# Kernel optimization log

Hardware: AMD Instinct MI355X
Metric: run time of the kernel (lower is better)

The kernel has to match this reference:

```python
import jax, jax.numpy as jnp
import numpy as np
from jax import lax

B_SZ = 2
EMBED = 384          # d_model == d_inner (expand=1)
DEPTH = 12
DSTATE = 16
DCONV = 4
DTRANK = 24          # ceil(384/16)
GH, GW, GD = 16, 8, 8
PH, PW, PD = 16, 32, 8
L = GH * GW * GD            # 1024 tokens
PATCH_DIM = PH * PW * PD    # 4096


def setup_inputs() -> dict:
    key = jax.random.key(0)
    ks = jax.random.split(key, 12)
    d = EMBED
    return {
        "x": jax.random.normal(ks[0], (B_SZ, 1, GH * PH, GW * PW, GD * PD), dtype=jnp.float32),
        "batch_params": jax.random.uniform(ks[1], (B_SZ, 4), minval=0.1, maxval=1.0),
        "patch_w": jax.random.normal(ks[2], (PATCH_DIM, d)) * 0.02,
        "patch_b": jnp.zeros((d,), jnp.float32),
        "in_proj_w": jax.random.normal(ks[3], (DEPTH, d, 2 * d)) * 0.02,
        "conv_w": jax.random.normal(ks[4], (DEPTH, d, DCONV)) * 0.1,
        "conv_b": jnp.zeros((DEPTH, d), jnp.float32),
        "x_proj_w": jax.random.normal(ks[5], (DEPTH, d, DTRANK + 2 * DSTATE)) * 0.02,
        "dt_proj_w": jax.random.normal(ks[6], (DEPTH, DTRANK, d)) * 0.02,
        "dt_proj_b": jnp.full((DEPTH, d), -4.6, jnp.float32),  # softplus(-4.6) ~ 0.01 init dt
        "A_log": jnp.log(jnp.tile(jnp.arange(1, DSTATE + 1, dtype=jnp.float32), (DEPTH, EMBED, 1))),
        "Dskip": jnp.ones((DEPTH, d), jnp.float32),
        "out_proj_w": jax.random.normal(ks[7], (DEPTH, d, d)) * 0.02,
        "norm_w": jnp.ones((DEPTH, d), jnp.float32),
        "norm_b": jnp.zeros((DEPTH, d), jnp.float32),
        "final_norm_w": jnp.ones((d,), jnp.float32),
        "final_norm_b": jnp.zeros((d,), jnp.float32),
        "has_velocity_mask": jnp.array([True, False]),
    }


def _layernorm(h, w, b, eps=1e-5):
    mu = h.mean(-1, keepdims=True)
    var = ((h - mu) ** 2).mean(-1, keepdims=True)
    return (h - mu) / jnp.sqrt(var + eps) * w + b


def _physical_coords(batch_params, mask):
    # grid indices -> physical (distance, angle, velocity/time), [B, L, 3]
    h = jnp.arange(GH, dtype=jnp.float32)[None, :, None, None]
    w = jnp.arange(GW, dtype=jnp.float32)[None, None, :, None]
    dd = jnp.arange(GD, dtype=jnp.float32)[None, None, None, :]
    rr = batch_params[:, 0][:, None, None, None]
    ar = batch_params[:, 1][:, None, None, None]
    vr = batch_params[:, 2][:, None, None, None]
    B = batch_params.shape[0]
    shape = (B, GH, GW, GD)
    dist = jnp.broadcast_to(h * rr, shape)
    angle = jnp.broadcast_to((w - GW / 2) * ar, shape)
    m = mask[:, None, None, None]
    vel = jnp.broadcast_to(jnp.where(m, (dd - GD / 2) * vr, dd * vr), shape)
    coords = jnp.stack([dist, angle, vel], axis=-1).reshape(B, -1, 3)
    # PIPE normalization
    d0 = coords[:, :, 0]
    dmax = jnp.max(d0, 1, keepdims=True)
    n0 = d0 / jnp.where(dmax == 0, 1.0, dmax)
    a = coords[:, :, 1]
    amax = jnp.max(jnp.abs(a), 1, keepdims=True)
    n1 = a / jnp.where(amax == 0, 1.0, amax)
    v = coords[:, :, 2]
    vam = jnp.max(jnp.abs(v), 1, keepdims=True)
    vam = jnp.where(vam == 0, 1.0, vam)
    vm = jnp.max(v, 1, keepdims=True)
    vm = jnp.where(vm == 0, 1.0, vm)
    n2 = jnp.where(mask[:, None], v / vam, v / vm)
    return jnp.stack([n0, n1, n2], axis=-1)


def _pos_embed(coords):
    # embed_dim % 3 == 0 and per-coord dim even -> pure sin/cos blocks
    dpc = EMBED // 3
    omega = 1.0 / (10000.0 ** (jnp.arange(dpc // 2, dtype=jnp.float32) / (dpc / 2.0)))
    embs = []
    for j in range(3):
        out = coords[:, :, j, None] * omega          # [B, L, dpc//2]
        embs.append(jnp.concatenate([jnp.sin(out), jnp.cos(out)], axis=-1))
    return jnp.concatenate(embs, axis=-1)            # [B, L, EMBED]


def _forward(x, batch_params, patch_w, patch_b, in_proj_w, conv_w, conv_b,
             x_proj_w, dt_proj_w, dt_proj_b, A_log, Dskip, out_proj_w,
             norm_w, norm_b, final_norm_w, final_norm_b, has_velocity_mask):
    B = x.shape[0]
    # 3D patch embed (conv3d with stride == kernel == patch) as reshape + GEMM
    xp = x[:, 0].reshape(B, GH, PH, GW, PW, GD, PD)
    xp = xp.transpose(0, 1, 3, 5, 2, 4, 6).reshape(B, L, PATCH_DIM)
    tok = xp @ patch_w + patch_b                     # [B, L, EMBED]
    coords = _physical_coords(batch_params, has_velocity_mask)
    tok = tok + _pos_embed(coords)

    def mamba_layer(tok, params):
        ipw, cw, cb, xpw, dtw, dtb, Al, Dp, opw, nw, nb = params
        h = _layernorm(tok, nw, nb)
        xz = h @ ipw                                  # [B, L, 2d]
        xi, z = jnp.split(xz, 2, axis=-1)
        # depthwise causal conv1d (kernel DCONV) + silu
        xc = lax.conv_general_dilated(
            xi.transpose(0, 2, 1), cw[:, None, :], (1,), [(DCONV - 1, 0)],
            feature_group_count=EMBED, dimension_numbers=("NCH", "OIH", "NCH"))
        xc = jax.nn.silu(xc + cb[:, None]).transpose(0, 2, 1)   # [B, L, d]
        dbl = xc @ xpw
        dt = jax.nn.softplus(dbl[..., :DTRANK] @ dtw + dtb)     # [B, L, d]
        Bm = dbl[..., DTRANK:DTRANK + DSTATE]                   # [B, L, N]
        Cm = dbl[..., DTRANK + DSTATE:]                         # [B, L, N]
        A = -jnp.exp(Al)                                        # [d, N]

        def step(hst, inps):
            dt_t, B_t, C_t, u_t = inps                          # [B,d],[B,N],[B,N],[B,d]
            dA = jnp.exp(dt_t[:, :, None] * A)                  # [B, d, N]
            hst = hst * dA + (dt_t * u_t)[:, :, None] * B_t[:, None, :]
            return hst, jnp.einsum("bdn,bn->bd", hst, C_t)

        h0 = jnp.zeros((B, EMBED, DSTATE), tok.dtype)
        _, ys = lax.scan(step, h0, (dt.transpose(1, 0, 2), Bm.transpose(1, 0, 2),
                                    Cm.transpose(1, 0, 2), xc.transpose(1, 0, 2)))
        y = ys.transpose(1, 0, 2) + xc * Dp
        y = y * jax.nn.silu(z)
        return tok + y @ opw, None

    tok, _ = lax.scan(mamba_layer, tok,
                      (in_proj_w, conv_w, conv_b, x_proj_w, dt_proj_w, dt_proj_b,
                       A_log, Dskip, out_proj_w, norm_w, norm_b))
    return _layernorm(tok, final_norm_w, final_norm_b)


def reference(x, batch_params, patch_w, patch_b, in_proj_w, conv_w, conv_b,
              x_proj_w, dt_proj_w, dt_proj_b, A_log, Dskip, out_proj_w,
              norm_w, norm_b, final_norm_w, final_norm_b, has_velocity_mask):
    return _forward(x, batch_params, patch_w, patch_b, in_proj_w, conv_w, conv_b,
                    x_proj_w, dt_proj_w, dt_proj_b, A_log, Dskip, out_proj_w,
                    norm_w, norm_b, final_norm_w, final_norm_b, has_velocity_mask)
```

## Files before the change

kernel.cpp:

```cpp
#include <hip/hip_runtime.h>


#define NTOK 2048

typedef short bf16x8 __attribute__((ext_vector_type(8)));
typedef float f32x4 __attribute__((ext_vector_type(4)));
typedef unsigned short us4 __attribute__((ext_vector_type(4)));

__device__ __forceinline__ float bf2f(unsigned short u) {
    return __uint_as_float(((unsigned)u) << 16);
}
__device__ __forceinline__ unsigned short f2bf(float f) {
    unsigned u = __float_as_uint(f);
    u += 0x7fffu + ((u >> 16) & 1u);
    return (unsigned short)(u >> 16);
}
__device__ __forceinline__ float siluf(float x) { return x / (1.f + expf(-x)); }

__device__ __forceinline__ float ldr(const void* p, size_t i, int bf) {
    if (bf) return bf2f(((const unsigned short*)p)[i]);
    return ((const float*)p)[i];
}
template<int BF>
__device__ __forceinline__ float ld(const void* p, size_t i) {
    if (BF) return bf2f(((const unsigned short*)p)[i]);
    return ((const float*)p)[i];
}

__global__ void detect_kernel(const void* dskip, int* flag) {
    flag[0] = (((const unsigned short*)dskip)[0] == 0x3F80u) ? 1 : 0;
}

__global__ __launch_bounds__(256)
void transposeP_kernel(const int* flag, const void* pw, unsigned short* wtP)
{
    __shared__ unsigned short Ts[32 * 36];
    const int bid = blockIdx.x;
    const int kb = bid / 12, nb = bid % 12;
    const int tid = threadIdx.x;
    const int r = tid >> 3, c0 = (tid & 7) * 4;
    const int BF = *flag;
#pragma unroll
    for (int i = 0; i < 4; i++) {
        size_t si = (size_t)(kb * 32 + r) * 384 + nb * 32 + c0 + i;
        Ts[(c0 + i) * 36 + r] = f2bf(ldr(pw, si, BF));
    }
    __syncthreads();
    *(us4*)(wtP + (size_t)(nb * 32 + r) * 4096 + kb * 32 + c0) = *(const us4*)&Ts[r * 36 + c0];
}

__global__ __launch_bounds__(256)
void transposeL_kernel(const int* flag, const void* ipw, const void* opw, int lyr,
                       unsigned short* wtL, unsigned short* wtOl)
{
    __shared__ unsigned short Ts[32 * 36];
    const int bid = blockIdx.x;
    const void* src; size_t soff; unsigned short* dst; int N, kb, nb;
    if (bid < 288) {
        src = ipw; soff = (size_t)lyr * 294912; dst = wtL; N = 768;
        kb = bid / 24; nb = bid % 24;
    } else {
        int rel = bid - 288;
        src = opw; soff = (size_t)lyr * 147456; dst = wtOl; N = 384;
        kb = rel / 12; nb = rel % 12;
    }
    const int tid = threadIdx.x;
    const int r = tid >> 3, c0 = (tid & 7) * 4;
    const int BF = *flag;
#pragma unroll
    for (int i = 0; i < 4; i++) {
        size_t si = soff + (size_t)(kb * 32 + r) * N + nb * 32 + c0 + i;
        Ts[(c0 + i) * 36 + r] = f2bf(ldr(src, si, BF));
    }
    __syncthreads();
    *(us4*)(dst + (size_t)(nb * 32 + r) * 384 + kb * 32 + c0) = *(const us4*)&Ts[r * 36 + c0];
}

__global__ __launch_bounds__(256)
void transposeAll_kernel(const int* flag, const void* ipw, const void* opw,
                         unsigned short* wtL12, unsigned short* wtO12)
{
    __shared__ unsigned short Ts[32 * 36];
    const int lyr = blockIdx.y;
    const int bid = blockIdx.x;
    const void* src; size_t soff; unsigned short* dst; int N, kb, nb;
    if (bid < 288) {
        src = ipw; soff = (size_t)lyr * 294912;
        dst = wtL12 + (size_t)lyr * 294912; N = 768;
        kb = bid / 24; nb = bid % 24;
    } else {
        int rel = bid - 288;
        src = opw; soff = (size_t)lyr * 147456;
        dst = wtO12 + (size_t)lyr * 147456; N = 384;
        kb = rel / 12; nb = rel % 12;
    }
    const int tid = threadIdx.x;
    const int r = tid >> 3, c0 = (tid & 7) * 4;
    const int BF = *flag;
#pragma unroll
    for (int i = 0; i < 4; i++) {
        size_t si = soff + (size_t)(kb * 32 + r) * N + nb * 32 + c0 + i;
        Ts[(c0 + i) * 36 + r] = f2bf(ldr(src, si, BF));
    }
    __syncthreads();
    *(us4*)(dst + (size_t)(nb * 32 + r) * 384 + kb * 32 + c0) = *(const us4*)&Ts[r * 36 + c0];
}


template<int MODE>
__global__ __launch_bounds__(256)
void gemm_kernel(const unsigned short* __restrict__ A,
                 const unsigned short* __restrict__ WT,
                 void* __restrict__ out0, unsigned short* __restrict__ out1)
{
    const int mtile = blockIdx.x;
    const int ntile = blockIdx.y;
    const int tid = threadIdx.x;
    const int w = tid >> 6, lane = tid & 63;
    const int l15 = lane & 15, quad = lane >> 4;
    const int mbase = mtile * 64 + (w & 1) * 32;
    const int nbase = ntile * 64 + (w >> 1) * 32;
    f32x4 acc00 = {0.f,0.f,0.f,0.f}, acc01 = acc00, acc10 = acc00, acc11 = acc00;
    const bf16x8* Ap0 = (const bf16x8*)(A + (size_t)(mbase + l15) * 384 + quad * 8);
    const bf16x8* Ap1 = (const bf16x8*)(A + (size_t)(mbase + 16 + l15) * 384 + quad * 8);
    const bf16x8* Bp0 = (const bf16x8*)(WT + (size_t)(nbase + l15) * 384 + quad * 8);
    const bf16x8* Bp1 = (const bf16x8*)(WT + (size_t)(nbase + 16 + l15) * 384 + quad * 8);
    const int nkt = (MODE == 1) ? 6 : 12;
    const int kt0 = (MODE == 1) ? blockIdx.z * 6 : 0;
#pragma unroll
    for (int ki = 0; ki < nkt; ki++) {
        const int kt = kt0 + ki;
        bf16x8 a0 = Ap0[kt * 4];
        bf16x8 a1 = Ap1[kt * 4];
        bf16x8 b0 = Bp0[kt * 4];
        bf16x8 b1 = Bp1[kt * 4];
        acc00 = __builtin_amdgcn_mfma_f32_16x16x32_bf16(a0, b0, acc00, 0, 0, 0);
        acc01 = __builtin_amdgcn_mfma_f32_16x16x32_bf16(a0, b1, acc01, 0, 0, 0);
        acc10 = __builtin_amdgcn_mfma_f32_16x16x32_bf16(a1, b0, acc10, 0, 0, 0);
        acc11 = __builtin_amdgcn_mfma_f32_16x16x32_bf16(a1, b1, acc11, 0, 0, 0);
    }
    f32x4 accs[2][2] = {{acc00, acc01}, {acc10, acc11}};
#pragma unroll
    for (int mi = 0; mi < 2; mi++)
#pragma unroll
    for (int ni = 0; ni < 2; ni++)
#pragma unroll
    for (int r = 0; r < 4; r++) {
        int m = mbase + mi * 16 + quad * 4 + r;
        int n = nbase + ni * 16 + l15;
        float v = accs[mi][ni][r];
        if (MODE == 0) {
            if (n < 384) ((unsigned short*)out0)[(size_t)m * 384 + n] = f2bf(v);
            else out1[(size_t)m * 384 + (n - 384)] = f2bf(siluf(v));
        } else {
            atomicAdd(&((float*)out0)[(size_t)m * 384 + n], v);
        }
    }
}

template<int BF>
__device__ void posinit_body(const void* __restrict__ pb, const void* __restrict__ bparams,
                             const unsigned char* __restrict__ maskp, float* __restrict__ tok)
{
    const int gid = blockIdx.x * 256 + threadIdx.x;
    const int t = gid / 384;
    const int n = gid - t * 384;
    const int b = t >> 10, l = t & 1023;
    const int gh = l >> 6, gw = (l >> 3) & 7, gd = l & 7;
    const int j = n >> 7;
    const int ii = n & 127;
    const int i0 = (ii < 64) ? ii : ii - 64;
    const float omega = exp2f(-(float)i0 * 0.20762050593046014f);
    float rr = ld<BF>(bparams, b * 4 + 0);
    float ar = ld<BF>(bparams, b * 4 + 1);
    float vr = ld<BF>(bparams, b * 4 + 2);
    bool mk = maskp[b] != 0;
    float cj;
    if (j == 0) {
        float dmax = (rr >= 0.f) ? 15.f * rr : 0.f;
        if (dmax == 0.f) dmax = 1.f;
        cj = (float)gh * rr / dmax;
    } else if (j == 1) {
        float amax = 4.f * fabsf(ar);
        if (amax == 0.f) amax = 1.f;
        cj = (float)(gw - 4) * ar / amax;
    } else {
        if (mk) {
            float dmx = 4.f * fabsf(vr);
            if (dmx == 0.f) dmx = 1.f;
            cj = (float)(gd - 4) * vr / dmx;
        } else {
            float dmx = (vr >= 0.f) ? 7.f * vr : 0.f;
            if (dmx == 0.f) dmx = 1.f;
            cj = (float)gd * vr / dmx;
        }
    }
    float s = cj * omega;
    float pos = (ii < 64) ? sinf(s) : cosf(s);
    tok[gid] = ld<BF>(pb, n) + pos;
}

__global__ __launch_bounds__(256)
void posinit_kernel(const int* flag, const void* pb, const void* bparams,
                    const unsigned char* maskp, float* tok)
{
    if (*flag) posinit_body<1>(pb, bparams, maskp, tok);
    else       posinit_body<0>(pb, bparams, maskp, tok);
}

template<int BF>
__device__ void patch_body(const void* __restrict__ x,
                           const unsigned short* __restrict__ WT,
                           float* __restrict__ tok, short* __restrict__ As)
{
    const int mtile = blockIdx.x;
    const int ntile = blockIdx.y;
    const int kz = blockIdx.z;
    const int tid = threadIdx.x;
    const int w = tid >> 6, lane = tid & 63;
    const int l15 = lane & 15, quad = lane >> 4;
    const int nbase = ntile * 64 + (w >> 1) * 32;
    const int mrow0 = (w & 1) * 32 + l15;
    f32x4 acc00 = {0.f,0.f,0.f,0.f}, acc01 = acc00, acc10 = acc00, acc11 = acc00;
#pragma unroll
    for (int p2 = 0; p2 < 2; p2++) {
        const int plane = kz * 2 + p2;
        if (p2) __syncthreads();
        {
            const int pw = lane >> 1;
            const int pd4 = (lane & 1) * 4;
#pragma unroll
            for (int i = 0; i < 16; i++) {
                int r = i * 4 + w;
                int t = mtile * 64 + r;
                int bb = t >> 10, l = t & 1023;
                int gh = l >> 6, gw = (l >> 3) & 7, gd = l & 7;
                size_t base = (size_t)bb * 4194304u + (size_t)gh * 262144u
                            + (size_t)gw * 2048u + (size_t)gd * 8u
                            + (size_t)plane * 16384u + (size_t)pw * 64u + (size_t)pd4;
                short* dst = As + r * 260 + lane * 4;
                if (BF) {
                    *(us4*)dst = *(const us4*)((const unsigned short*)x + base);
                } else {
                    float4 p4 = *(const float4*)((const float*)x + base);
                    dst[0] = (short)f2bf(p4.x); dst[1] = (short)f2bf(p4.y);
                    dst[2] = (short)f2bf(p4.z); dst[3] = (short)f2bf(p4.w);
                }
            }
        }
        __syncthreads();
        const bf16x8* Bp0 = (const bf16x8*)(WT + (size_t)(nbase + l15) * 4096
                                            + plane * 256 + quad * 8);
        const bf16x8* Bp1 = (const bf16x8*)(WT + (size_t)(nbase + 16 + l15) * 4096
                                            + plane * 256 + quad * 8);
#pragma unroll
        for (int kt = 0; kt < 8; kt++) {
            const short* a0p = As + mrow0 * 260 + kt * 32 + quad * 8;
            const short* a1p = a0p + 16 * 260;
            bf16x8 a0, a1;
            {
                us4 lo = *(const us4*)a0p, hi = *(const us4*)(a0p + 4);
                a0[0]=lo[0]; a0[1]=lo[1]; a0[2]=lo[2]; a0[3]=lo[3];
                a0[4]=hi[0]; a0[5]=hi[1]; a0[6]=hi[2]; a0[7]=hi[3];
                us4 lo1 = *(const us4*)a1p, hi1 = *(const us4*)(a1p + 4);
                a1[0]=lo1[0]; a1[1]=lo1[1]; a1[2]=lo1[2]; a1[3]=lo1[3];
                a1[4]=hi1[0]; a1[5]=hi1[1]; a1[6]=hi1[2]; a1[7]=hi1[3];
            }
            bf16x8 b0 = Bp0[kt * 4];
            bf16x8 b1 = Bp1[kt * 4];
            acc00 = __builtin_amdgcn_mfma_f32_16x16x32_bf16(a0, b0, acc00, 0, 0, 0);
            acc01 = __builtin_amdgcn_mfma_f32_16x16x32_bf16(a0, b1, acc01, 0, 0, 0);
            acc10 = __builtin_amdgcn_mfma_f32_16x16x32_bf16(a1, b0, acc10, 0, 0, 0);
            acc11 = __builtin_amdgcn_mfma_f32_16x16x32_bf16(a1, b1, acc11, 0, 0, 0);
        }
    }
    f32x4 accs[2][2] = {{acc00, acc01}, {acc10, acc11}};
#pragma unroll
    for (int mi = 0; mi < 2; mi++)
#pragma unroll
    for (int ni = 0; ni < 2; ni++) {
        int n = nbase + ni * 16 + l15;
#pragma unroll
        for (int r = 0; r < 4; r++) {
            int m = mtile * 64 + (w & 1) * 32 + mi * 16 + quad * 4 + r;
            atomicAdd(&tok[(size_t)m * 384 + n], accs[mi][ni][r]);
        }
    }
}

__global__ __launch_bounds__(256)
void patch_kernel(const int* flag, const void* x, const unsigned short* wtP, float* tok)
{
    __shared__ short As[64 * 260];
    if (*flag) patch_body<1>(x, wtP, tok, As);
    else       patch_body<0>(x, wtP, tok, As);
}

__global__ __launch_bounds__(64)
void ln_kernel(const int* flag, const float* __restrict__ in, const void* __restrict__ w,
               const void* __restrict__ b, int woff, void* __restrict__ out, int obf)
{
    const int BF = *flag;
    const int wbf = obf | BF;
    const int t = blockIdx.x;
    const int lane = threadIdx.x;
    float v[6];
    float s = 0.f;
#pragma unroll
    for (int i = 0; i < 6; i++) { v[i] = in[(size_t)t * 384 + lane + 64 * i]; s += v[i]; }
#pragma unroll
    for (int o = 1; o < 64; o <<= 1) s += __shfl_xor(s, o);
    const float mu = s * (1.f / 384.f);
    float s2 = 0.f;
#pragma unroll
    for (int i = 0; i < 6; i++) { float d = v[i] - mu; s2 += d * d; }
#pragma unroll
    for (int o = 1; o < 64; o <<= 1) s2 += __shfl_xor(s2, o);
    const float rstd = rsqrtf(s2 * (1.f / 384.f) + 1e-5f);
#pragma unroll
    for (int i = 0; i < 6; i++) {
        int c = lane + 64 * i;
        float o = (v[i] - mu) * rstd * ldr(w, woff + c, BF) + ldr(b, woff + c, BF);
        if (wbf) ((unsigned short*)out)[(size_t)t * 384 + c] = f2bf(o);
        else     ((float*)out)[(size_t)t * 384 + c] = o;
    }
}

template<int BF>
__device__ void convfused_body(float* xcs, float* dblA,
                          const unsigned short* __restrict__ xi,
                          const void* __restrict__ cw, const void* __restrict__ cb,
                          const void* __restrict__ xpw, const void* __restrict__ dtw,
                          const void* __restrict__ dtbp, int lyr,
                          unsigned short* __restrict__ xc, unsigned short* __restrict__ dtv,
                          float* __restrict__ Bm, float* __restrict__ Cm)
{
    const int tb = blockIdx.x * 4;
    const int tid = threadIdx.x;
    const size_t cwo = (size_t)lyr * 1536;
    const size_t cbo = (size_t)lyr * 384;
    const size_t xpo = (size_t)lyr * 21504;
    const size_t dto = (size_t)lyr * 9216;
#pragma unroll
    for (int i = 0; i < 6; i++) {
        int p = i * 256 + tid;
        int tl = p / 384, c = p - tl * 384;
        int t = tb + tl;
        int b = t >> 10, l = t & 1023;
        float acc = ld<BF>(cb, cbo + c);
#pragma unroll
        for (int jj = 0; jj < 4; jj++) {
            int ls = l - 3 + jj;
            if (ls >= 0)
                acc = fmaf(bf2f(xi[(size_t)((b << 10) + ls) * 384 + c]),
                           ld<BF>(cw, cwo + c * 4 + jj), acc);
        }
        float s = siluf(acc);
        xcs[tl * 384 + c] = s;
        xc[(size_t)t * 384 + c] = f2bf(s);
    }
    __syncthreads();
    {
        const int tok = tid >> 6, og = tid & 63;
        const int t = tb + tok;
        if (og < 56) {
            float acc = 0.f;
            const float* xr = xcs + tok * 384;
#pragma unroll 8
            for (int k = 0; k < 384; k++)
                acc = fmaf(xr[k], ld<BF>(xpw, xpo + (size_t)k * 56 + og), acc);
            if (og < 24) dblA[tok * 24 + og] = acc;
            else if (og < 40) Bm[(size_t)t * 16 + (og - 24)] = acc;
            else Cm[(size_t)t * 16 + (og - 40)] = acc;
        }
    }
    __syncthreads();
#pragma unroll
    for (int i = 0; i < 6; i++) {
        int p = i * 256 + tid;
        int tl = p / 384, c = p - tl * 384;
        int t = tb + tl;
        float acc = ld<BF>(dtbp, cbo + c);
        const float* dr = dblA + tl * 24;
#pragma unroll
        for (int r = 0; r < 24; r++)
            acc = fmaf(dr[r], ld<BF>(dtw, dto + (size_t)r * 384 + c), acc);
        float sp = fmaxf(acc, 0.f) + log1pf(expf(-fabsf(acc)));
        dtv[(size_t)t * 384 + c] = f2bf(sp);
    }
}

__global__ __launch_bounds__(256)
void convfused_kernel(const int* flag, const unsigned short* xi, const void* cw,
                      const void* cb, const void* xpw, const void* dtw, const void* dtbp,
                      int lyr, unsigned short* xc, unsigned short* dtv,
                      float* Bm, float* Cm)
{
    __shared__ float xcs[4 * 384];
    __shared__ float dblA[4 * 24];
    if (*flag) convfused_body<1>(xcs, dblA, xi, cw, cb, xpw, dtw, dtbp, lyr, xc, dtv, Bm, Cm);
    else       convfused_body<0>(xcs, dblA, xi, cw, cb, xpw, dtw, dtbp, lyr, xc, dtv, Bm, Cm);
}

template<int BF>
__device__ void scan1_body(unsigned short* dts, unsigned short* xcs, float* Bs,
                           const unsigned short* __restrict__ dt,
                           const unsigned short* __restrict__ xc,
                           const float* __restrict__ Bm, const void* __restrict__ Alog,
                           int aoff, float* __restrict__ chA, float* __restrict__ chH)
{
    const int b = blockIdx.z, ch = blockIdx.y;
    const int tid = threadIdx.x;
    const int cl = tid >> 4;
    const int c = blockIdx.x * 16 + cl;
    const int n = tid & 15;
    const int tbase = (b << 10) + ch * 64;
    {
        const int row = tid >> 2, part = (tid & 3) * 4;
        const int c0 = blockIdx.x * 16;
        *(us4*)&dts[row * 16 + part] =
            *(const us4*)(dt + (size_t)(tbase + row) * 384 + c0 + part);
        *(us4*)&xcs[row * 16 + part] =
            *(const us4*)(xc + (size_t)(tbase + row) * 384 + c0 + part);
        *(float4*)&Bs[tid * 4] = *(const float4*)(Bm + (size_t)tbase * 16 + tid * 4);
    }
    __syncthreads();
    const float Ac = -expf(ld<BF>(Alog, (size_t)aoff + c * 16 + n));
    float h = 0.f, ap = 1.f;
#pragma unroll 4
    for (int i = 0; i < 64; i++) {
        float d = bf2f(dts[i * 16 + cl]);
        float u = bf2f(xcs[i * 16 + cl]);
        float bn = Bs[i * 16 + n];
        float dA = expf(d * Ac);
        h = fmaf(h, dA, d * u * bn);
        ap *= dA;
    }
    size_t idx = ((size_t)((b * 16 + ch) * 384 + c)) * 16 + n;
    chA[idx] = ap;
    chH[idx] = h;
}

__global__ __launch_bounds__(256)
void scan1_kernel(const int* flag, const unsigned short* dt, const unsigned short* xc,
                  const float* Bm, const void* Alog, int aoff, float* chA, float* chH)
{
    __shared__ unsigned short dts[1024];
    __shared__ unsigned short xcs[1024];
    __shared__ float Bs[1024];
    if (*flag) scan1_body<1>(dts, xcs, Bs, dt, xc, Bm, Alog, aoff, chA, chH);
    else       scan1_body<0>(dts, xcs, Bs, dt, xc, Bm, Alog, aoff, chA, chH);
}

template<int BF>
__device__ void scan2_body(unsigned short* dts, unsigned short* xcs, unsigned short* zss,
                           float* Bs, float* Cs,
                           const unsigned short* __restrict__ dt,
                           const unsigned short* __restrict__ xc,
                           const float* __restrict__ Bm, const float* __restrict__ Cm,
                           const unsigned short* __restrict__ zs,
                           const void* __restrict__ Alog, const void* __restrict__ Dp,
                           int aoff, int doff,
                           const float* __restrict__ chA, const float* __restrict__ chH,
                           unsigned short* __restrict__ y)
{
    const int b = blockIdx.z, ch = blockIdx.y;
    const int tid = threadIdx.x;
    const int cl = tid >> 4;
    const int c = blockIdx.x * 16 + cl;
    const int n = tid & 15;
    const int tbase = (b << 10) + ch * 64;
    {
        const int row = tid >> 2, part = (tid & 3) * 4;
        const int c0 = blockIdx.x * 16;
        *(us4*)&dts[row * 16 + part] =
            *(const us4*)(dt + (size_t)(tbase + row) * 384 + c0 + part);
        *(us4*)&xcs[row * 16 + part] =
            *(const us4*)(xc + (size_t)(tbase + row) * 384 + c0 + part);
        *(us4*)&zss[row * 16 + part] =
            *(const us4*)(zs + (size_t)(tbase + row) * 384 + c0 + part);
        *(float4*)&Bs[tid * 4] = *(const float4*)(Bm + (size_t)tbase * 16 + tid * 4);
        *(float4*)&Cs[tid * 4] = *(const float4*)(Cm + (size_t)tbase * 16 + tid * 4);
    }
    const float Ac = -expf(ld<BF>(Alog, (size_t)aoff + c * 16 + n));
    const float dp = ld<BF>(Dp, (size_t)doff + c);
    float h = 0.f;
    for (int c2 = 0; c2 < ch; c2++) {
        size_t i2 = ((size_t)((b * 16 + c2) * 384 + c)) * 16 + n;
        h = fmaf(chA[i2], h, chH[i2]);
    }
    __syncthreads();
#pragma unroll 4
    for (int i = 0; i < 64; i++) {
        float d = bf2f(dts[i * 16 + cl]);
        float u = bf2f(xcs[i * 16 + cl]);
        float bn = Bs[i * 16 + n];
        float cn = Cs[i * 16 + n];
        float dA = expf(d * Ac);
        h = fmaf(h, dA, d * u * bn);
        float p = h * cn;
        p += __shfl_xor(p, 1);
        p += __shfl_xor(p, 2);
        p += __shfl_xor(p, 4);
        p += __shfl_xor(p, 8);
        if (n == 0) {
            int t = tbase + i;
            y[(size_t)t * 384 + c] = f2bf((p + u * dp) * bf2f(zss[i * 16 + cl]));
        }
    }
}

__global__ __launch_bounds__(256)
void scan2_kernel(const int* flag, const unsigned short* dt, const unsigned short* xc,
                  const float* Bm, const float* Cm, const unsigned short* zs,
                  const void* Alog, const void* Dp, int aoff, int doff,
                  const float* chA, const float* chH, unsigned short* y)
{
    __shared__ unsigned short dts[1024];
    __shared__ unsigned short xcs[1024];
    __shared__ unsigned short zss[1024];
    __shared__ float Bs[1024];
    __shared__ float Cs[1024];
    if (*flag) scan2_body<1>(dts, xcs, zss, Bs, Cs, dt, xc, Bm, Cm, zs, Alog, Dp,
                             aoff, doff, chA, chH, y);
    else       scan2_body<0>(dts, xcs, zss, Bs, Cs, dt, xc, Bm, Cm, zs, Alog, Dp,
                             aoff, doff, chA, chH, y);
}

extern "C" void kernel_launch(void* const* d_in, const int* in_sizes, int n_in,
                              void* d_out, int out_size, void* d_ws, size_t ws_size,
                              hipStream_t stream) {
    const void* x        = d_in[0];
    const void* bparams  = d_in[1];
    const void* patch_w  = d_in[2];
    const void* patch_b  = d_in[3];
    const void* in_proj  = d_in[4];
    const void* conv_w   = d_in[5];
    const void* conv_b   = d_in[6];
    const void* x_proj   = d_in[7];
    const void* dt_w     = d_in[8];
    const void* dt_b     = d_in[9];
    const void* A_log    = d_in[10];
    const void* Dskip    = d_in[11];
    const void* out_proj = d_in[12];
    const void* norm_w   = d_in[13];
    const void* norm_b   = d_in[14];
    const void* fnw      = d_in[15];
    const void* fnb      = d_in[16];
    const unsigned char* maskp = (const unsigned char*)d_in[17];

    const size_t TD = (size_t)NTOK * 384;
    char* p = (char*)d_ws;
    float* tok = (float*)p;              p += TD * 4;
    unsigned short* hbuf = (unsigned short*)p; p += TD * 2;
    unsigned short* xi   = (unsigned short*)p; p += TD * 2;
    unsigned short* zs   = (unsigned short*)p; p += TD * 2;
    unsigned short* xc   = (unsigned short*)p; p += TD * 2;
    unsigned short* dtb_ = (unsigned short*)p; p += TD * 2;
    float* Bmb = (float*)p;              p += (size_t)NTOK * 16 * 4;
    float* Cmb = (float*)p;              p += (size_t)NTOK * 16 * 4;
    float* chA = (float*)p;              p += 196608 * 4;
    float* chH = (float*)p;              p += 196608 * 4;
    int* dflag = (int*)p;                p += 256;
    unsigned short* wbase = (unsigned short*)p;
    const size_t fixed = (size_t)(p - (char*)d_ws);
    const int big = (ws_size >= fixed + (size_t)(12 * 294912 + 12 * 147456) * 2 + 4096);

    unsigned short* wtP   = wbase;
    unsigned short* wtL12 = wbase;
    unsigned short* wtO12 = wbase + (size_t)12 * 294912;
    unsigned short* wtLs  = wbase + (size_t)1572864;
    unsigned short* wtOs  = wtLs + (size_t)294912;
    unsigned short* yb    = hbuf;

    detect_kernel<<<1, 1, 0, stream>>>(Dskip, dflag);
    transposeP_kernel<<<1536, 256, 0, stream>>>(dflag, patch_w, wtP);
    posinit_kernel<<<3072, 256, 0, stream>>>(dflag, patch_b, bparams, maskp, tok);
    patch_kernel<<<dim3(32, 6, 8), 256, 0, stream>>>(dflag, x, wtP, tok);
    if (big)
        transposeAll_kernel<<<dim3(432, 12), 256, 0, stream>>>(dflag, in_proj, out_proj,
                                                               wtL12, wtO12);

    for (int lyr = 0; lyr < 12; lyr++) {
        unsigned short *wtL, *wtO;
        if (big) {
            wtL = wtL12 + (size_t)lyr * 294912;
            wtO = wtO12 + (size_t)lyr * 147456;
        } else {
            transposeL_kernel<<<432, 256, 0, stream>>>(dflag, in_proj, out_proj, lyr,
                                                       wtLs, wtOs);
            wtL = wtLs; wtO = wtOs;
        }
        ln_kernel<<<NTOK, 64, 0, stream>>>(dflag, tok, norm_w, norm_b, lyr * 384, hbuf, 1);
        gemm_kernel<0><<<dim3(32, 12), 256, 0, stream>>>(hbuf, wtL, xi, zs);
        convfused_kernel<<<NTOK / 4, 256, 0, stream>>>(
            dflag, xi, conv_w, conv_b, x_proj, dt_w, dt_b, lyr, xc, dtb_, Bmb, Cmb);
        scan1_kernel<<<dim3(24, 16, 2), 256, 0, stream>>>(
            dflag, dtb_, xc, Bmb, A_log, lyr * 384 * 16, chA, chH);
        scan2_kernel<<<dim3(24, 16, 2), 256, 0, stream>>>(
            dflag, dtb_, xc, Bmb, Cmb, zs, A_log, Dskip, lyr * 384 * 16, lyr * 384,
            chA, chH, yb);
        gemm_kernel<1><<<dim3(32, 6, 2), 256, 0, stream>>>(yb, wtO, tok, nullptr);
    }

    ln_kernel<<<NTOK, 64, 0, stream>>>(dflag, tok, fnw, fnb, 0, d_out, 0);
}
```

Baseline: 1.251 ms.

## Fuse per-layer LayerNorm into in_proj GEMM and retile patch embedding GEMM

Adds an lngemm kernel that loads each 64-token tile of the residual stream, computes LayerNorm statistics in one pass, writes normalized bf16 rows to shared memory, and runs the in_proj MFMA GEMM from there. This removes the separate ln_kernel launch and the hbuf round trip in every layer. The catch is that each of the 12 N-tiles recomputes LayerNorm for the same rows, and variance now comes from E[x^2]-mu^2, which is less numerically stable. Separately, the patch-embedding kernel is retiled so each block covers 32 tokens across all 384 outputs. That cuts the repeated loading and conversion of x tiles across N-tiles, at the cost of more accumulator registers.

```diff
diff --git a/kernel.cpp b/kernel.cpp
--- a/kernel.cpp
+++ b/kernel.cpp
@@ -106,7 +106,6 @@
     *(us4*)(dst + (size_t)(nb * 32 + r) * 384 + kb * 32 + c0) = *(const us4*)&Ts[r * 36 + c0];
 }
 
-
 template<int MODE>
 __global__ __launch_bounds__(256)
 void gemm_kernel(const unsigned short* __restrict__ A,
@@ -155,6 +154,88 @@
         } else {
             atomicAdd(&((float*)out0)[(size_t)m * 384 + n], v);
         }
+    }
+}
+
+__global__ __launch_bounds__(256)
+void lngemm_kernel(const int* flag, const float* __restrict__ tok,
+                   const void* __restrict__ nw, const void* __restrict__ nb, int woff,
+                   const unsigned short* __restrict__ WT,
+                   unsigned short* __restrict__ xi, unsigned short* __restrict__ zs)
+{
+    __shared__ short As[64 * 392];
+    const int BF = *flag;
+    const int mtile = blockIdx.x;
+    const int ntile = blockIdx.y;
+    const int tid = threadIdx.x;
+    const int w = tid >> 6, lane = tid & 63;
+    const int l15 = lane & 15, quad = lane >> 4;
+    {
+        const int row = w * 16 + (lane >> 2);
+        const int sub = lane & 3;
+        const float* src = tok + (size_t)(mtile * 64 + row) * 384 + sub * 96;
+        float s = 0.f, s2 = 0.f;
+#pragma unroll
+        for (int j = 0; j < 24; j++) {
+            float4 p = ((const float4*)src)[j];
+            s += p.x + p.y + p.z + p.w;
+            s2 += p.x * p.x + p.y * p.y + p.z * p.z + p.w * p.w;
+        }
+        s  += __shfl_xor(s, 1);  s  += __shfl_xor(s, 2);
+        s2 += __shfl_xor(s2, 1); s2 += __shfl_xor(s2, 2);
+        const float mu = s * (1.f / 384.f);
+        const float rstd = rsqrtf(fmaxf(s2 * (1.f / 384.f) - mu * mu, 0.f) + 1e-5f);
+        short* dst = As + row * 392 + sub * 96;
+#pragma unroll
+        for (int j = 0; j < 24; j++) {
+            float4 p = ((const float4*)src)[j];
+            int c = woff + sub * 96 + j * 4;
+            us4 o;
+            o[0] = f2bf((p.x - mu) * rstd * ldr(nw, c + 0, BF) + ldr(nb, c + 0, BF));
+            o[1] = f2bf((p.y - mu) * rstd * ldr(nw, c + 1, BF) + ldr(nb, c + 1, BF));
+            o[2] = f2bf((p.z - mu) * rstd * ldr(nw, c + 2, BF) + ldr(nb, c + 2, BF));
+            o[3] = f2bf((p.w - mu) * rstd * ldr(nw, c + 3, BF) + ldr(nb, c + 3, BF));
+            *(us4*)(dst + j * 4) = o;
+        }
+    }
+    __syncthreads();
+    const int mloc = (w & 1) * 32;
+    const int nbase = ntile * 64 + (w >> 1) * 32;
+    f32x4 acc00 = {0.f,0.f,0.f,0.f}, acc01 = acc00, acc10 = acc00, acc11 = acc00;
+    const bf16x8* Bp0 = (const bf16x8*)(WT + (size_t)(nbase + l15) * 384 + quad * 8);
+    const bf16x8* Bp1 = (const bf16x8*)(WT + (size_t)(nbase + 16 + l15) * 384 + quad * 8);
+#pragma unroll
+    for (int kt = 0; kt < 12; kt++) {
+        const short* a0p = As + (mloc + l15) * 392 + kt * 32 + quad * 8;
+        const short* a1p = a0p + 16 * 392;
+        bf16x8 a0, a1;
+        {
+            us4 lo = *(const us4*)a0p, hi = *(const us4*)(a0p + 4);
+            a0[0]=lo[0]; a0[1]=lo[1]; a0[2]=lo[2]; a0[3]=lo[3];
+            a0[4]=hi[0]; a0[5]=hi[1]; a0[6]=hi[2]; a0[7]=hi[3];
+            us4 lo1 = *(const us4*)a1p, hi1 = *(const us4*)(a1p + 4);
+            a1[0]=lo1[0]; a1[1]=lo1[1]; a1[2]=lo1[2]; a1[3]=lo1[3];
+            a1[4]=hi1[0]; a1[5]=hi1[1]; a1[6]=hi1[2]; a1[7]=hi1[3];
+        }
+        bf16x8 b0 = Bp0[kt * 4];
+        bf16x8 b1 = Bp1[kt * 4];
+        acc00 = __builtin_amdgcn_mfma_f32_16x16x32_bf16(a0, b0, acc00, 0, 0, 0);
+        acc01 = __builtin_amdgcn_mfma_f32_16x16x32_bf16(a0, b1, acc01, 0, 0, 0);
+        acc10 = __builtin_amdgcn_mfma_f32_16x16x32_bf16(a1, b0, acc10, 0, 0, 0);
+        acc11 = __builtin_amdgcn_mfma_f32_16x16x32_bf16(a1, b1, acc11, 0, 0, 0);
+    }
+    f32x4 accs[2][2] = {{acc00, acc01}, {acc10, acc11}};
+#pragma unroll
+    for (int mi = 0; mi < 2; mi++)
+#pragma unroll
+    for (int ni = 0; ni < 2; ni++)
+#pragma unroll
+    for (int r = 0; r < 4; r++) {
+        int m = mtile * 64 + mloc + mi * 16 + quad * 4 + r;
+        int n = nbase + ni * 16 + l15;
+        float v = accs[mi][ni][r];
+        if (n < 384) xi[(size_t)m * 384 + n] = f2bf(v);
+        else zs[(size_t)m * 384 + (n - 384)] = f2bf(siluf(v));
     }
 }
 
@@ -213,15 +294,17 @@
                            const unsigned short* __restrict__ WT,
                            float* __restrict__ tok, short* __restrict__ As)
 {
-    const int mtile = blockIdx.x;
-    const int ntile = blockIdx.y;
-    const int kz = blockIdx.z;
+    const int mt = blockIdx.x;
+    const int kz = blockIdx.y;
     const int tid = threadIdx.x;
     const int w = tid >> 6, lane = tid & 63;
     const int l15 = lane & 15, quad = lane >> 4;
-    const int nbase = ntile * 64 + (w >> 1) * 32;
-    const int mrow0 = (w & 1) * 32 + l15;
-    f32x4 acc00 = {0.f,0.f,0.f,0.f}, acc01 = acc00, acc10 = acc00, acc11 = acc00;
+    f32x4 acc[2][6];
+#pragma unroll
+    for (int mi = 0; mi < 2; mi++)
+#pragma unroll
+    for (int nj = 0; nj < 6; nj++)
+        acc[mi][nj] = (f32x4){0.f, 0.f, 0.f, 0.f};
 #pragma unroll
     for (int p2 = 0; p2 < 2; p2++) {
         const int plane = kz * 2 + p2;
@@ -230,9 +313,9 @@
             const int pw = lane >> 1;
             const int pd4 = (lane & 1) * 4;
 #pragma unroll
-            for (int i = 0; i < 16; i++) {
+            for (int i = 0; i < 8; i++) {
                 int r = i * 4 + w;
-                int t = mtile * 64 + r;
+                int t = mt * 32 + r;
                 int bb = t >> 10, l = t & 1023;
                 int gh = l >> 6, gw = (l >> 3) & 7, gd = l & 7;
                 size_t base = (size_t)bb * 4194304u + (size_t)gh * 262144u
@@ -249,16 +332,14 @@
             }
         }
         __syncthreads();
-        const bf16x8* Bp0 = (const bf16x8*)(WT + (size_t)(nbase + l15) * 4096
-                                            + plane * 256 + quad * 8);
-        const bf16x8* Bp1 = (const bf16x8*)(WT + (size_t)(nbase + 16 + l15) * 4096
-                                            + plane * 256 + quad * 8);
+        const unsigned short* Bbase = WT + (size_t)(w * 96 + l15) * 4096
+                                    + plane * 256 + quad * 8;
 #pragma unroll
         for (int kt = 0; kt < 8; kt++) {
-            const short* a0p = As + mrow0 * 260 + kt * 32 + quad * 8;
-            const short* a1p = a0p + 16 * 260;
             bf16x8 a0, a1;
             {
+                const short* a0p = As + l15 * 260 + kt * 32 + quad * 8;
+                const short* a1p = a0p + 16 * 260;
                 us4 lo = *(const us4*)a0p, hi = *(const us4*)(a0p + 4);
                 a0[0]=lo[0]; a0[1]=lo[1]; a0[2]=lo[2]; a0[3]=lo[3];
                 a0[4]=hi[0]; a0[5]=hi[1]; a0[6]=hi[2]; a0[7]=hi[3];
@@ -266,24 +347,23 @@
                 a1[0]=lo1[0]; a1[1]=lo1[1]; a1[2]=lo1[2]; a1[3]=lo1[3];
                 a1[4]=hi1[0]; a1[5]=hi1[1]; a1[6]=hi1[2]; a1[7]=hi1[3];
             }
-            bf16x8 b0 = Bp0[kt * 4];
-            bf16x8 b1 = Bp1[kt * 4];
-            acc00 = __builtin_amdgcn_mfma_f32_16x16x32_bf16(a0, b0, acc00, 0, 0, 0);
-            acc01 = __builtin_amdgcn_mfma_f32_16x16x32_bf16(a0, b1, acc01, 0, 0, 0);
-            acc10 = __builtin_amdgcn_mfma_f32_16x16x32_bf16(a1, b0, acc10, 0, 0, 0);
-            acc11 = __builtin_amdgcn_mfma_f32_16x16x32_bf16(a1, b1, acc11, 0, 0, 0);
-        }
-    }
-    f32x4 accs[2][2] = {{acc00, acc01}, {acc10, acc11}};
+#pragma unroll
+            for (int nj = 0; nj < 6; nj++) {
+                bf16x8 b = *(const bf16x8*)(Bbase + (size_t)nj * 65536 + kt * 32);
+                acc[0][nj] = __builtin_amdgcn_mfma_f32_16x16x32_bf16(a0, b, acc[0][nj], 0, 0, 0);
+                acc[1][nj] = __builtin_amdgcn_mfma_f32_16x16x32_bf16(a1, b, acc[1][nj], 0, 0, 0);
+            }
+        }
+    }
 #pragma unroll
     for (int mi = 0; mi < 2; mi++)
 #pragma unroll
-    for (int ni = 0; ni < 2; ni++) {
-        int n = nbase + ni * 16 + l15;
+    for (int nj = 0; nj < 6; nj++) {
+        int n = w * 96 + nj * 16 + l15;
 #pragma unroll
         for (int r = 0; r < 4; r++) {
-            int m = mtile * 64 + (w & 1) * 32 + mi * 16 + quad * 4 + r;
-            atomicAdd(&tok[(size_t)m * 384 + n], accs[mi][ni][r]);
+            int m = mt * 32 + mi * 16 + quad * 4 + r;
+            atomicAdd(&tok[(size_t)m * 384 + n], acc[mi][nj][r]);
         }
     }
 }
@@ -291,7 +371,7 @@
 __global__ __launch_bounds__(256)
 void patch_kernel(const int* flag, const void* x, const unsigned short* wtP, float* tok)
 {
-    __shared__ short As[64 * 260];
+    __shared__ short As[32 * 260];
     if (*flag) patch_body<1>(x, wtP, tok, As);
     else       patch_body<0>(x, wtP, tok, As);
 }
@@ -576,7 +656,7 @@
     detect_kernel<<<1, 1, 0, stream>>>(Dskip, dflag);
     transposeP_kernel<<<1536, 256, 0, stream>>>(dflag, patch_w, wtP);
     posinit_kernel<<<3072, 256, 0, stream>>>(dflag, patch_b, bparams, maskp, tok);
-    patch_kernel<<<dim3(32, 6, 8), 256, 0, stream>>>(dflag, x, wtP, tok);
+    patch_kernel<<<dim3(64, 8), 256, 0, stream>>>(dflag, x, wtP, tok);
     if (big)
         transposeAll_kernel<<<dim3(432, 12), 256, 0, stream>>>(dflag, in_proj, out_proj,
                                                                wtL12, wtO12);
@@ -591,8 +671,8 @@
                                                        wtLs, wtOs);
             wtL = wtLs; wtO = wtOs;
         }
-        ln_kernel<<<NTOK, 64, 0, stream>>>(dflag, tok, norm_w, norm_b, lyr * 384, hbuf, 1);
-        gemm_kernel<0><<<dim3(32, 12), 256, 0, stream>>>(hbuf, wtL, xi, zs);
+        lngemm_kernel<<<dim3(32, 12), 256, 0, stream>>>(
+            dflag, tok, norm_w, norm_b, lyr * 384, wtL, xi, zs);
         convfused_kernel<<<NTOK / 4, 256, 0, stream>>>(
             dflag, xi, conv_w, conv_b, x_proj, dt_w, dt_b, lyr, xc, dtb_, Bmb, Cmb);
         scan1_kernel<<<dim3(24, 16, 2), 256, 0, stream>>>(
```

New measurement: 1.378 ms. 1.1x slower.

## Fuse two-pass chunked selective scan into one cooperative kernel with grid sync

Applied to the files above, without the earlier changes.

Merges the chunk-local scan pass and the chunk-combine/output pass into a single cooperative kernel that uses a grid-wide barrier between them. Each block keeps its dt, xc, B, C and z tiles in shared memory across both phases, which removes one launch and the reload of those tiles. The cost is a cooperative launch and a grid.sync, and the 768-block grid must be fully co-resident on the device or the launch fails.

```diff
diff --git a/kernel.cpp b/kernel.cpp
--- a/kernel.cpp
+++ b/kernel.cpp
@@ -1,4 +1,7 @@
 #include <hip/hip_runtime.h>
+#include <hip/hip_cooperative_groups.h>
+
+namespace cg = cooperative_groups;
 
 
 #define NTOK 2048
@@ -105,7 +108,6 @@
     __syncthreads();
     *(us4*)(dst + (size_t)(nb * 32 + r) * 384 + kb * 32 + c0) = *(const us4*)&Ts[r * 36 + c0];
 }
-
 
 template<int MODE>
 __global__ __launch_bounds__(256)
@@ -403,66 +405,17 @@
 }
 
 template<int BF>
-__device__ void scan1_body(unsigned short* dts, unsigned short* xcs, float* Bs,
-                           const unsigned short* __restrict__ dt,
-                           const unsigned short* __restrict__ xc,
-                           const float* __restrict__ Bm, const void* __restrict__ Alog,
-                           int aoff, float* __restrict__ chA, float* __restrict__ chH)
-{
-    const int b = blockIdx.z, ch = blockIdx.y;
-    const int tid = threadIdx.x;
-    const int cl = tid >> 4;
-    const int c = blockIdx.x * 16 + cl;
-    const int n = tid & 15;
-    const int tbase = (b << 10) + ch * 64;
-    {
-        const int row = tid >> 2, part = (tid & 3) * 4;
-        const int c0 = blockIdx.x * 16;
-        *(us4*)&dts[row * 16 + part] =
-            *(const us4*)(dt + (size_t)(tbase + row) * 384 + c0 + part);
-        *(us4*)&xcs[row * 16 + part] =
-            *(const us4*)(xc + (size_t)(tbase + row) * 384 + c0 + part);
-        *(float4*)&Bs[tid * 4] = *(const float4*)(Bm + (size_t)tbase * 16 + tid * 4);
-    }
-    __syncthreads();
-    const float Ac = -expf(ld<BF>(Alog, (size_t)aoff + c * 16 + n));
-    float h = 0.f, ap = 1.f;
-#pragma unroll 4
-    for (int i = 0; i < 64; i++) {
-        float d = bf2f(dts[i * 16 + cl]);
-        float u = bf2f(xcs[i * 16 + cl]);
-        float bn = Bs[i * 16 + n];
-        float dA = expf(d * Ac);
-        h = fmaf(h, dA, d * u * bn);
-        ap *= dA;
-    }
-    size_t idx = ((size_t)((b * 16 + ch) * 384 + c)) * 16 + n;
-    chA[idx] = ap;
-    chH[idx] = h;
-}
-
-__global__ __launch_bounds__(256)
-void scan1_kernel(const int* flag, const unsigned short* dt, const unsigned short* xc,
-                  const float* Bm, const void* Alog, int aoff, float* chA, float* chH)
-{
-    __shared__ unsigned short dts[1024];
-    __shared__ unsigned short xcs[1024];
-    __shared__ float Bs[1024];
-    if (*flag) scan1_body<1>(dts, xcs, Bs, dt, xc, Bm, Alog, aoff, chA, chH);
-    else       scan1_body<0>(dts, xcs, Bs, dt, xc, Bm, Alog, aoff, chA, chH);
-}
-
-template<int BF>
-__device__ void scan2_body(unsigned short* dts, unsigned short* xcs, unsigned short* zss,
-                           float* Bs, float* Cs,
-                           const unsigned short* __restrict__ dt,
-                           const unsigned short* __restrict__ xc,
-                           const float* __restrict__ Bm, const float* __restrict__ Cm,
-                           const unsigned short* __restrict__ zs,
-                           const void* __restrict__ Alog, const void* __restrict__ Dp,
-                           int aoff, int doff,
-                           const float* __restrict__ chA, const float* __restrict__ chH,
-                           unsigned short* __restrict__ y)
+__device__ void scanfused_body(unsigned short* dts, unsigned short* xcs,
+                               unsigned short* zss, float* Bs, float* Cs,
+                               cg::grid_group& grid,
+                               const unsigned short* __restrict__ dt,
+                               const unsigned short* __restrict__ xc,
+                               const float* __restrict__ Bm, const float* __restrict__ Cm,
+                               const unsigned short* __restrict__ zs,
+                               const void* __restrict__ Alog, const void* __restrict__ Dp,
+                               int aoff, int doff,
+                               float* __restrict__ chA, float* __restrict__ chH,
+                               unsigned short* __restrict__ y)
 {
     const int b = blockIdx.z, ch = blockIdx.y;
     const int tid = threadIdx.x;
@@ -482,14 +435,28 @@
         *(float4*)&Bs[tid * 4] = *(const float4*)(Bm + (size_t)tbase * 16 + tid * 4);
         *(float4*)&Cs[tid * 4] = *(const float4*)(Cm + (size_t)tbase * 16 + tid * 4);
     }
+    __syncthreads();
     const float Ac = -expf(ld<BF>(Alog, (size_t)aoff + c * 16 + n));
     const float dp = ld<BF>(Dp, (size_t)doff + c);
-    float h = 0.f;
+    float h = 0.f, ap = 1.f;
+#pragma unroll 4
+    for (int i = 0; i < 64; i++) {
+        float d = bf2f(dts[i * 16 + cl]);
+        float u = bf2f(xcs[i * 16 + cl]);
+        float bn = Bs[i * 16 + n];
+        float dA = expf(d * Ac);
+        h = fmaf(h, dA, d * u * bn);
+        ap *= dA;
+    }
+    size_t idx = ((size_t)((b * 16 + ch) * 384 + c)) * 16 + n;
+    chA[idx] = ap;
+    chH[idx] = h;
+    grid.sync();
+    float h2 = 0.f;
     for (int c2 = 0; c2 < ch; c2++) {
         size_t i2 = ((size_t)((b * 16 + c2) * 384 + c)) * 16 + n;
-        h = fmaf(chA[i2], h, chH[i2]);
-    }
-    __syncthreads();
+        h2 = fmaf(chA[i2], h2, chH[i2]);
+    }
 #pragma unroll 4
     for (int i = 0; i < 64; i++) {
         float d = bf2f(dts[i * 16 + cl]);
@@ -497,8 +464,8 @@
         float bn = Bs[i * 16 + n];
         float cn = Cs[i * 16 + n];
         float dA = expf(d * Ac);
-        h = fmaf(h, dA, d * u * bn);
-        float p = h * cn;
+        h2 = fmaf(h2, dA, d * u * bn);
+        float p = h2 * cn;
         p += __shfl_xor(p, 1);
         p += __shfl_xor(p, 2);
         p += __shfl_xor(p, 4);
@@ -511,20 +478,21 @@
 }
 
 __global__ __launch_bounds__(256)
-void scan2_kernel(const int* flag, const unsigned short* dt, const unsigned short* xc,
-                  const float* Bm, const float* Cm, const unsigned short* zs,
-                  const void* Alog, const void* Dp, int aoff, int doff,
-                  const float* chA, const float* chH, unsigned short* y)
+void scanfused_kernel(const int* flag, const unsigned short* dt, const unsigned short* xc,
+                      const float* Bm, const float* Cm, const unsigned short* zs,
+                      const void* Alog, const void* Dp, int aoff, int doff,
+                      float* chA, float* chH, unsigned short* y)
 {
     __shared__ unsigned short dts[1024];
     __shared__ unsigned short xcs[1024];
     __shared__ unsigned short zss[1024];
     __shared__ float Bs[1024];
     __shared__ float Cs[1024];
-    if (*flag) scan2_body<1>(dts, xcs, zss, Bs, Cs, dt, xc, Bm, Cm, zs, Alog, Dp,
-                             aoff, doff, chA, chH, y);
-    else       scan2_body<0>(dts, xcs, zss, Bs, Cs, dt, xc, Bm, Cm, zs, Alog, Dp,
-                             aoff, doff, chA, chH, y);
+    cg::grid_group grid = cg::this_grid();
+    if (*flag) scanfused_body<1>(dts, xcs, zss, Bs, Cs, grid, dt, xc, Bm, Cm, zs,
+                                 Alog, Dp, aoff, doff, chA, chH, y);
+    else       scanfused_body<0>(dts, xcs, zss, Bs, Cs, grid, dt, xc, Bm, Cm, zs,
+                                 Alog, Dp, aoff, doff, chA, chH, y);
 }
 
 extern "C" void kernel_launch(void* const* d_in, const int* in_sizes, int n_in,
@@ -595,11 +563,25 @@
         gemm_kernel<0><<<dim3(32, 12), 256, 0, stream>>>(hbuf, wtL, xi, zs);
         convfused_kernel<<<NTOK / 4, 256, 0, stream>>>(
             dflag, xi, conv_w, conv_b, x_proj, dt_w, dt_b, lyr, xc, dtb_, Bmb, Cmb);
-        scan1_kernel<<<dim3(24, 16, 2), 256, 0, stream>>>(
-            dflag, dtb_, xc, Bmb, A_log, lyr * 384 * 16, chA, chH);
-        scan2_kernel<<<dim3(24, 16, 2), 256, 0, stream>>>(
-            dflag, dtb_, xc, Bmb, Cmb, zs, A_log, Dskip, lyr * 384 * 16, lyr * 384,
-            chA, chH, yb);
+        {
+            int aoff = lyr * 384 * 16, doff = lyr * 384;
+            const int* fl = dflag;
+            const unsigned short* a_dt = dtb_;
+            const unsigned short* a_xc = xc;
+            const float* a_Bm = Bmb;
+            const float* a_Cm = Cmb;
+            const unsigned short* a_zs = zs;
+            const void* a_Al = A_log;
+            const void* a_Dp = Dskip;
+            float* a_chA = chA;
+            float* a_chH = chH;
+            unsigned short* a_y = yb;
+            void* args[] = { &fl, &a_dt, &a_xc, &a_Bm, &a_Cm, &a_zs, &a_Al, &a_Dp,
+                             &aoff, &doff, &a_chA, &a_chH, &a_y };
+            hipLaunchCooperativeKernel((const void*)scanfused_kernel,
+                                       dim3(24, 16, 2), dim3(256, 1, 1),
+                                       args, 0, stream);
+        }
         gemm_kernel<1><<<dim3(32, 6, 2), 256, 0, stream>>>(yb, wtO, tok, nullptr);
     }
 
```

After: 2.563 ms. +105.0%, slower.
